# Kernel optimization log

Hardware: AMD Instinct MI355X
Metric: run time of the kernel (lower is better)

Reference implementation:

```python
import jax, jax.numpy as jnp
import numpy as np

EMB = 128
HID = 128
N = 1024


def setup_inputs() -> dict:
    key = jax.random.key(0)
    ks = jax.random.split(key, 10)
    s1 = 1.0 / np.sqrt(2 * EMB)
    s2 = 1.0 / np.sqrt(HID)
    return {
        "z1": jax.random.normal(ks[0], (N, EMB), jnp.float32),
        "z2": jax.random.normal(ks[1], (N, EMB), jnp.float32),
        "W1": jax.random.uniform(ks[2], (HID, 2 * EMB), jnp.float32, -s1, s1),
        "b1": jax.random.uniform(ks[3], (HID,), jnp.float32, -s1, s1),
        "W2": jax.random.uniform(ks[4], (HID, HID), jnp.float32, -s2, s2),
        "b2": jax.random.uniform(ks[5], (HID,), jnp.float32, -s2, s2),
        "W3": jax.random.uniform(ks[6], (1, HID), jnp.float32, -s2, s2),
        "b3": jax.random.uniform(ks[7], (1,), jnp.float32, -s2, s2),
    }


def reference(z1, z2, W1, b1, W2, b2, W3, b3):
    # pairs[i, j] = concat(z1[j], z2[i]); first Linear split into two matmuls
    # so the [n, n, 2*emb] concat tensor is never materialized (same math).
    W1a = W1[:, :EMB]   # acts on z1 half
    W1b = W1[:, EMB:]   # acts on z2 half
    a = jnp.einsum('jd,hd->jh', z1, W1a)          # [n, h], varies along j
    b = jnp.einsum('id,hd->ih', z2, W1b)          # [n, h], varies along i
    h1 = jax.nn.gelu(a[None, :, :] + b[:, None, :] + b1, approximate=False)  # [n, n, h]
    h2 = jax.nn.gelu(jnp.einsum('ijh,gh->ijg', h1, W2) + b2, approximate=False)
    log_q = jnp.einsum('ijh,oh->ijo', h2, W3) + b3  # [n, n, 1]
    return log_q[..., 0]
```

## Files before the change

kernel.cpp:

```cpp
#include <hip/hip_runtime.h>

#define NN  1024
#define EMB 128
#define HID 128

typedef __attribute__((ext_vector_type(4))) float float4v;
typedef __attribute__((ext_vector_type(8))) float float8v;
typedef __attribute__((ext_vector_type(8))) short short8;
typedef __attribute__((ext_vector_type(4))) __bf16 bf16x4;
typedef __attribute__((ext_vector_type(8))) __bf16 bf16x8;

__device__ __forceinline__ short8 to_bf16x8(float4v a, float4v b) {
  float8v f = {a[0], a[1], a[2], a[3], b[0], b[1], b[2], b[3]};
  bf16x8 r = __builtin_convertvector(f, bf16x8);
  return __builtin_bit_cast(short8, r);
}

__device__ __forceinline__ void store_bf16x4(short* p, float4v v) {
  bf16x4 r = __builtin_convertvector(v, bf16x4);
  *(bf16x4*)p = r;
}

__device__ __forceinline__ float4v gelu4(float4v x) {
  float4v x2 = x * x;
  float4v t = x2 * 0.1029432f + 2.3022086f;
  float4v y = x * t;
  float4v e;
  e[0] = __builtin_amdgcn_exp2f(y[0]);
  e[1] = __builtin_amdgcn_exp2f(y[1]);
  e[2] = __builtin_amdgcn_exp2f(y[2]);
  e[3] = __builtin_amdgcn_exp2f(y[3]);
  float4v d = e + 1.0f;
  float p01 = d[0] * d[1];
  float p23 = d[2] * d[3];
  float rall = __builtin_amdgcn_rcpf(p01 * p23);
  float r01 = p23 * rall;
  float r23 = p01 * rall;
  float4v rv;
  rv[0] = d[1] * r01;
  rv[1] = d[0] * r01;
  rv[2] = d[3] * r23;
  rv[3] = d[2] * r23;
  return x - x * rv;
}

__device__ __forceinline__ float4v mfma16(short8 a, short8 b, float4v c) {
  return __builtin_amdgcn_mfma_f32_16x16x32_bf16(a, b, c, 0, 0, 0);
}

__global__ __launch_bounds__(256)
void prep_kernel(const float* __restrict__ z1, const float* __restrict__ z2,
                 const float* __restrict__ W1, const float* __restrict__ b1,
                 const float* __restrict__ W2,
                 float* __restrict__ Abuf, float* __restrict__ Bbuf,
                 unsigned short* __restrict__ W2f) {
  int blk = blockIdx.x, tid = threadIdx.x;
  if (blk < 256) {
    int which = blk >> 7;
    int j0 = ((blk & 127) >> 1) << 4;
    int hh = blk & 1;
    const float* z = which ? z2 : z1;
    __shared__ __align__(16) short zf[4 * 64 * 8];
    __shared__ __align__(16) short w1f[16 * 64 * 8];

#pragma unroll
    for (int p = 0; p < 2; ++p) {
      int u = p * 256 + tid;
      int row = u >> 5;
      int c = (u & 31) * 4;
      float4v v = *(const float4v*)(z + (j0 + row) * EMB + c);
      int kt = c >> 5;
      int lane = ((c >> 3) & 3) * 16 + row;
      store_bf16x4(zf + (kt * 64 + lane) * 8 + (c & 7), v);
    }
    {
      const float* wbase = W1 + (hh * 64) * (2 * EMB) + which * EMB;
#pragma unroll
      for (int p = 0; p < 8; ++p) {
        int u = p * 256 + tid;
        int grow = u >> 5;
        int c = (u & 31) * 4;
        float4v v = *(const float4v*)(wbase + grow * (2 * EMB) + c);
        int kt = c >> 5;
        int ntl = grow >> 4;
        int lane = ((c >> 3) & 3) * 16 + (grow & 15);
        store_bf16x4(w1f + ((kt * 4 + ntl) * 64 + lane) * 8 + (c & 7), v);
      }
    }
    __syncthreads();

    int w = tid >> 6, l = tid & 63, r = l & 15, q = l >> 4;
    float4v acc = {};
#pragma unroll
    for (int kt = 0; kt < 4; ++kt) {
      short8 az = *(const short8*)(zf + (kt * 64 + l) * 8);
      short8 bf = *(const short8*)(w1f + ((kt * 4 + w) * 64 + l) * 8);
      acc = mfma16(az, bf, acc);
    }
    int gg = hh * 64 + w * 16 + r;
    float ba = which ? 0.0f : b1[gg];
    float* dstp = which ? Bbuf : Abuf;
#pragma unroll
    for (int reg = 0; reg < 4; ++reg)
      dstp[(j0 + q * 4 + reg) * HID + gg] = acc[reg] + ba;
  } else {
    int s0 = (blk - 256) * 2048 + tid * 8;
    float4v v0 = *(const float4v*)(W2 + s0);
    float4v v1 = *(const float4v*)(W2 + s0 + 4);
    float vals[8] = {v0[0], v0[1], v0[2], v0[3], v1[0], v1[1], v1[2], v1[3]};
#pragma unroll
    for (int j = 0; j < 8; ++j) {
      int s = s0 + j;
      int g = s >> 7;
      int h = s & 127;
      int kt = h >> 5;
      int nt = g >> 4;
      int lane = ((h >> 3) & 3) * 16 + (g & 15);
      int dst = ((kt * 8 + nt) * 64 + lane) * 8 + (h & 7);
      unsigned u = __float_as_uint(vals[j]);
      W2f[dst] = (unsigned short)((u + 0x7FFFu + ((u >> 16) & 1u)) >> 16);
    }
  }
}

__global__ __launch_bounds__(256, 4)
void fused_mlp_kernel(const float* __restrict__ Abuf, const float* __restrict__ Bbuf,
                      const float* __restrict__ W2f4,
                      const float* __restrict__ b2, const float* __restrict__ W3,
                      const float* __restrict__ b3, float* __restrict__ out) {
  __shared__ __align__(16) short s_w2[HID * HID];

  int tid = threadIdx.x;
  {
    const float4v* src = (const float4v*)W2f4;
    float4v* dst = (float4v*)s_w2;
#pragma unroll
    for (int t = 0; t < 8; ++t)
      dst[tid + t * 256] = src[tid + t * 256];
  }

  int w = tid >> 6, l = tid & 63, r = l & 15, q = l >> 4;
  int bi = (blockIdx.x >> 6) << 3;
  int bj = (blockIdx.x & 63) << 4;

  const float* Ap  = Abuf + (bj + r) * HID + q * 8;
  const float* Bp0 = Bbuf + (bi + 2 * w) * HID + q * 8;
  const float* Bp1 = Bp0 + HID;

  short8 afs[4][2];
  float4v s0 = {0.f, 0.f, 0.f, 0.f};
  float4v s1 = {0.f, 0.f, 0.f, 0.f};
  float4v acc[2][4];

  __syncthreads();

#pragma unroll
  for (int nt = 0; nt < 4; ++nt) {
    float4v bv = *(const float4v*)(b2 + nt * 16 + q * 4);
    acc[0][nt] = bv;
    acc[1][nt] = bv;
  }

  float4v a0  = *(const float4v*)(Ap);
  float4v a1  = *(const float4v*)(Ap + 4);
  float4v b00 = *(const float4v*)(Bp0);
  float4v b01 = *(const float4v*)(Bp0 + 4);
  float4v b10 = *(const float4v*)(Bp1);
  float4v b11 = *(const float4v*)(Bp1 + 4);

#pragma unroll
  for (int kt = 0; kt < 4; ++kt) {
    float4v ca0 = a0, ca1 = a1, cb00 = b00, cb01 = b01, cb10 = b10, cb11 = b11;
    if (kt < 3) {
      int off = (kt + 1) * 32;
      a0  = *(const float4v*)(Ap + off);
      a1  = *(const float4v*)(Ap + off + 4);
      b00 = *(const float4v*)(Bp0 + off);
      b01 = *(const float4v*)(Bp0 + off + 4);
      b10 = *(const float4v*)(Bp1 + off);
      b11 = *(const float4v*)(Bp1 + off + 4);
    }
    short8 af0 = to_bf16x8(gelu4(ca0 + cb00), gelu4(ca1 + cb01));
    short8 af1 = to_bf16x8(gelu4(ca0 + cb10), gelu4(ca1 + cb11));
    afs[kt][0] = af0;
    afs[kt][1] = af1;

    const short8* wrow = (const short8*)s_w2 + kt * 512 + l;
#pragma unroll
    for (int nt = 0; nt < 4; ++nt) {
      short8 wf = wrow[nt * 64];
      acc[0][nt] = mfma16(wf, af0, acc[0][nt]);
      acc[1][nt] = mfma16(wf, af1, acc[1][nt]);
    }
  }

#pragma unroll
  for (int nt = 0; nt < 4; ++nt) {
    float4v wv = *(const float4v*)(W3 + nt * 16 + q * 4);
    s0 = s0 + gelu4(acc[0][nt]) * wv;
    s1 = s1 + gelu4(acc[1][nt]) * wv;
  }

#pragma unroll
  for (int nt = 0; nt < 4; ++nt) {
    float4v bv = *(const float4v*)(b2 + (nt + 4) * 16 + q * 4);
    acc[0][nt] = bv;
    acc[1][nt] = bv;
  }
#pragma unroll
  for (int kt = 0; kt < 4; ++kt) {
    short8 af0 = afs[kt][0];
    short8 af1 = afs[kt][1];
    const short8* wrow = (const short8*)s_w2 + kt * 512 + 4 * 64 + l;
#pragma unroll
    for (int nt = 0; nt < 4; ++nt) {
      short8 wf = wrow[nt * 64];
      acc[0][nt] = mfma16(wf, af0, acc[0][nt]);
      acc[1][nt] = mfma16(wf, af1, acc[1][nt]);
    }
  }
#pragma unroll
  for (int nt = 0; nt < 4; ++nt) {
    float4v wv = *(const float4v*)(W3 + (nt + 4) * 16 + q * 4);
    s0 = s0 + gelu4(acc[0][nt]) * wv;
    s1 = s1 + gelu4(acc[1][nt]) * wv;
  }

  float bias3 = b3[0];
  float sc0 = s0[0] + s0[1] + s0[2] + s0[3];
  float sc1 = s1[0] + s1[1] + s1[2] + s1[3];
  sc0 += __shfl_xor(sc0, 16, 64);
  sc0 += __shfl_xor(sc0, 32, 64);
  sc1 += __shfl_xor(sc1, 16, 64);
  sc1 += __shfl_xor(sc1, 32, 64);
  if (l < 16) {
    out[(bi + 2 * w) * NN + bj + l]     = sc0 + bias3;
    out[(bi + 2 * w + 1) * NN + bj + l] = sc1 + bias3;
  }
}

extern "C" void kernel_launch(void* const* d_in, const int* in_sizes, int n_in,
                              void* d_out, int out_size, void* d_ws, size_t ws_size,
                              hipStream_t stream) {
  const float* z1 = (const float*)d_in[0];
  const float* z2 = (const float*)d_in[1];
  const float* W1 = (const float*)d_in[2];
  const float* b1 = (const float*)d_in[3];
  const float* W2 = (const float*)d_in[4];
  const float* b2 = (const float*)d_in[5];
  const float* W3 = (const float*)d_in[6];
  const float* b3 = (const float*)d_in[7];
  float* out = (float*)d_out;

  float* Abuf = (float*)d_ws;
  float* Bbuf = Abuf + NN * HID;
  unsigned short* W2f = (unsigned short*)(Bbuf + NN * HID);

  prep_kernel<<<264, 256, 0, stream>>>(z1, z2, W1, b1, W2, Abuf, Bbuf, W2f);
  fused_mlp_kernel<<<(NN / 8) * (NN / 16), 256, 0, stream>>>(
      Abuf, Bbuf, (const float*)W2f, b2, W3, b3, out);
}
```

Before: 160.9 us.

## Load W2 tiles straight into LDS and reorder W2 fragment layout by half

The W2 copy from global memory into shared memory now uses direct global-to-LDS loads instead of a register round-trip. The prep kernel lays out W2 fragments so that output columns 0-63 and 64-127 occupy separate contiguous halves, and the MLP kernel's indexing is updated to match. The manual software prefetch of the A/B activations is removed, leaving each k-step to load its own values. This trims registers and copy instructions and lets the first half of W2 be consumed on its own, at the cost of exposing activation load latency.

Result: no change. 158.9 us (-1.2%).

```diff
diff --git a/kernel.cpp b/kernel.cpp
--- a/kernel.cpp
+++ b/kernel.cpp
@@ -115,8 +115,9 @@
       int h = s & 127;
       int kt = h >> 5;
       int nt = g >> 4;
+      int p = nt >> 2;
       int lane = ((h >> 3) & 3) * 16 + (g & 15);
-      int dst = ((kt * 8 + nt) * 64 + lane) * 8 + (h & 7);
+      int dst = p * 8192 + ((kt * 4 + (nt & 3)) * 64 + lane) * 8 + (h & 7);
       unsigned u = __float_as_uint(vals[j]);
       W2f[dst] = (unsigned short)((u + 0x7FFFu + ((u >> 16) & 1u)) >> 16);
     }
@@ -131,15 +132,20 @@
   __shared__ __align__(16) short s_w2[HID * HID];
 
   int tid = threadIdx.x;
+  int w = tid >> 6, l = tid & 63, r = l & 15, q = l >> 4;
+
   {
-    const float4v* src = (const float4v*)W2f4;
-    float4v* dst = (float4v*)s_w2;
-#pragma unroll
-    for (int t = 0; t < 8; ++t)
-      dst[tid + t * 256] = src[tid + t * 256];
-  }
-
-  int w = tid >> 6, l = tid & 63, r = l & 15, q = l >> 4;
+    const float4v* wsrc = (const float4v*)W2f4;
+    int wb = tid & 192;
+#pragma unroll
+    for (int t = 0; t < 8; ++t) {
+      __builtin_amdgcn_global_load_lds(
+          (const __attribute__((address_space(1))) void*)(wsrc + t * 256 + tid),
+          (__attribute__((address_space(3))) void*)(s_w2 + (t * 256 + wb) * 8),
+          16, 0, 0);
+    }
+  }
+
   int bi = (blockIdx.x >> 6) << 3;
   int bj = (blockIdx.x & 63) << 4;
 
@@ -161,31 +167,22 @@
     acc[1][nt] = bv;
   }
 
-  float4v a0  = *(const float4v*)(Ap);
-  float4v a1  = *(const float4v*)(Ap + 4);
-  float4v b00 = *(const float4v*)(Bp0);
-  float4v b01 = *(const float4v*)(Bp0 + 4);
-  float4v b10 = *(const float4v*)(Bp1);
-  float4v b11 = *(const float4v*)(Bp1 + 4);
-
 #pragma unroll
   for (int kt = 0; kt < 4; ++kt) {
-    float4v ca0 = a0, ca1 = a1, cb00 = b00, cb01 = b01, cb10 = b10, cb11 = b11;
-    if (kt < 3) {
-      int off = (kt + 1) * 32;
-      a0  = *(const float4v*)(Ap + off);
-      a1  = *(const float4v*)(Ap + off + 4);
-      b00 = *(const float4v*)(Bp0 + off);
-      b01 = *(const float4v*)(Bp0 + off + 4);
-      b10 = *(const float4v*)(Bp1 + off);
-      b11 = *(const float4v*)(Bp1 + off + 4);
-    }
+    int off = kt * 32;
+    float4v ca0  = *(const float4v*)(Ap + off);
+    float4v ca1  = *(const float4v*)(Ap + off + 4);
+    float4v cb00 = *(const float4v*)(Bp0 + off);
+    float4v cb01 = *(const float4v*)(Bp0 + off + 4);
+    float4v cb10 = *(const float4v*)(Bp1 + off);
+    float4v cb11 = *(const float4v*)(Bp1 + off + 4);
+
     short8 af0 = to_bf16x8(gelu4(ca0 + cb00), gelu4(ca1 + cb01));
     short8 af1 = to_bf16x8(gelu4(ca0 + cb10), gelu4(ca1 + cb11));
     afs[kt][0] = af0;
     afs[kt][1] = af1;
 
-    const short8* wrow = (const short8*)s_w2 + kt * 512 + l;
+    const short8* wrow = (const short8*)s_w2 + kt * 256 + l;
 #pragma unroll
     for (int nt = 0; nt < 4; ++nt) {
       short8 wf = wrow[nt * 64];
@@ -211,7 +208,7 @@
   for (int kt = 0; kt < 4; ++kt) {
     short8 af0 = afs[kt][0];
     short8 af1 = afs[kt][1];
-    const short8* wrow = (const short8*)s_w2 + kt * 512 + 4 * 64 + l;
+    const short8* wrow = (const short8*)s_w2 + 1024 + kt * 256 + l;
 #pragma unroll
     for (int nt = 0; nt < 4; ++nt) {
       short8 wf = wrow[nt * 64];
```

## Load W2 into LDS via direct global_load_lds and pack GELU as float2 ops

Applied to the files above, without the earlier changes.

Replaces the register-staged copy of the pre-swizzled W2 fragments into shared memory with direct global-to-LDS loads, and reorders the W2 fragment layout in the prep kernel so each output-half's tiles are contiguous. The GELU helper and accumulators are restructured into float2 pieces so the compiler can emit packed FP32 instructions. The intent is to cut VGPR pressure and instruction count in the load prologue and the GELU-heavy inner loop. It relies on the per-wave LDS base addressing of global_load_lds matching the layout, and on the compiler actually emitting packed math.

Measured after the change: 157.3 us. 2.2% less time.

```diff
diff --git a/kernel.cpp b/kernel.cpp
--- a/kernel.cpp
+++ b/kernel.cpp
@@ -4,14 +4,18 @@
 #define EMB 128
 #define HID 128
 
+typedef __attribute__((ext_vector_type(2))) float float2v;
 typedef __attribute__((ext_vector_type(4))) float float4v;
 typedef __attribute__((ext_vector_type(8))) float float8v;
 typedef __attribute__((ext_vector_type(8))) short short8;
 typedef __attribute__((ext_vector_type(4))) __bf16 bf16x4;
 typedef __attribute__((ext_vector_type(8))) __bf16 bf16x8;
 
-__device__ __forceinline__ short8 to_bf16x8(float4v a, float4v b) {
-  float8v f = {a[0], a[1], a[2], a[3], b[0], b[1], b[2], b[3]};
+__device__ __forceinline__ float2v lo2(float4v v) { float2v r; r[0] = v[0]; r[1] = v[1]; return r; }
+__device__ __forceinline__ float2v hi2(float4v v) { float2v r; r[0] = v[2]; r[1] = v[3]; return r; }
+
+__device__ __forceinline__ short8 to_bf16x8_pk(float2v al, float2v ah, float2v bl, float2v bh) {
+  float8v f = {al[0], al[1], ah[0], ah[1], bl[0], bl[1], bh[0], bh[1]};
   bf16x8 r = __builtin_convertvector(f, bf16x8);
   return __builtin_bit_cast(short8, r);
 }
@@ -21,27 +25,33 @@
   *(bf16x4*)p = r;
 }
 
-__device__ __forceinline__ float4v gelu4(float4v x) {
-  float4v x2 = x * x;
-  float4v t = x2 * 0.1029432f + 2.3022086f;
-  float4v y = x * t;
-  float4v e;
-  e[0] = __builtin_amdgcn_exp2f(y[0]);
-  e[1] = __builtin_amdgcn_exp2f(y[1]);
-  e[2] = __builtin_amdgcn_exp2f(y[2]);
-  e[3] = __builtin_amdgcn_exp2f(y[3]);
-  float4v d = e + 1.0f;
-  float p01 = d[0] * d[1];
-  float p23 = d[2] * d[3];
+__device__ __forceinline__ void gelu4pk(float2v xl, float2v xh,
+                                        float2v& ol, float2v& oh) {
+  float2v x2l = xl * xl;
+  float2v x2h = xh * xh;
+  float2v tl = x2l * 0.1029432f + 2.3022086f;
+  float2v th = x2h * 0.1029432f + 2.3022086f;
+  float2v yl = xl * tl;
+  float2v yh = xh * th;
+  float2v el, eh;
+  el[0] = __builtin_amdgcn_exp2f(yl[0]);
+  el[1] = __builtin_amdgcn_exp2f(yl[1]);
+  eh[0] = __builtin_amdgcn_exp2f(yh[0]);
+  eh[1] = __builtin_amdgcn_exp2f(yh[1]);
+  float2v dl = el + 1.0f;
+  float2v dh = eh + 1.0f;
+  float p01 = dl[0] * dl[1];
+  float p23 = dh[0] * dh[1];
   float rall = __builtin_amdgcn_rcpf(p01 * p23);
   float r01 = p23 * rall;
   float r23 = p01 * rall;
-  float4v rv;
-  rv[0] = d[1] * r01;
-  rv[1] = d[0] * r01;
-  rv[2] = d[3] * r23;
-  rv[3] = d[2] * r23;
-  return x - x * rv;
+  float2v rvl, rvh;
+  rvl[0] = dl[1] * r01;
+  rvl[1] = dl[0] * r01;
+  rvh[0] = dh[1] * r23;
+  rvh[1] = dh[0] * r23;
+  ol = xl - xl * rvl;
+  oh = xh - xh * rvh;
 }
 
 __device__ __forceinline__ float4v mfma16(short8 a, short8 b, float4v c) {
@@ -115,8 +125,9 @@
       int h = s & 127;
       int kt = h >> 5;
       int nt = g >> 4;
+      int p = nt >> 2;
       int lane = ((h >> 3) & 3) * 16 + (g & 15);
-      int dst = ((kt * 8 + nt) * 64 + lane) * 8 + (h & 7);
+      int dst = p * 8192 + ((kt * 4 + (nt & 3)) * 64 + lane) * 8 + (h & 7);
       unsigned u = __float_as_uint(vals[j]);
       W2f[dst] = (unsigned short)((u + 0x7FFFu + ((u >> 16) & 1u)) >> 16);
     }
@@ -131,15 +142,20 @@
   __shared__ __align__(16) short s_w2[HID * HID];
 
   int tid = threadIdx.x;
+  int w = tid >> 6, l = tid & 63, r = l & 15, q = l >> 4;
+
   {
-    const float4v* src = (const float4v*)W2f4;
-    float4v* dst = (float4v*)s_w2;
-#pragma unroll
-    for (int t = 0; t < 8; ++t)
-      dst[tid + t * 256] = src[tid + t * 256];
-  }
-
-  int w = tid >> 6, l = tid & 63, r = l & 15, q = l >> 4;
+    const float4v* wsrc = (const float4v*)W2f4;
+    int wb = tid & 192;
+#pragma unroll
+    for (int t = 0; t < 8; ++t) {
+      __builtin_amdgcn_global_load_lds(
+          (const __attribute__((address_space(1))) void*)(wsrc + t * 256 + tid),
+          (__attribute__((address_space(3))) void*)(s_w2 + (t * 256 + wb) * 8),
+          16, 0, 0);
+    }
+  }
+
   int bi = (blockIdx.x >> 6) << 3;
   int bj = (blockIdx.x & 63) << 4;
 
@@ -148,8 +164,8 @@
   const float* Bp1 = Bp0 + HID;
 
   short8 afs[4][2];
-  float4v s0 = {0.f, 0.f, 0.f, 0.f};
-  float4v s1 = {0.f, 0.f, 0.f, 0.f};
+  float2v s0l = {0.f, 0.f}, s0h = {0.f, 0.f};
+  float2v s1l = {0.f, 0.f}, s1h = {0.f, 0.f};
   float4v acc[2][4];
 
   __syncthreads();
@@ -180,12 +196,17 @@
       b10 = *(const float4v*)(Bp1 + off);
       b11 = *(const float4v*)(Bp1 + off + 4);
     }
-    short8 af0 = to_bf16x8(gelu4(ca0 + cb00), gelu4(ca1 + cb01));
-    short8 af1 = to_bf16x8(gelu4(ca0 + cb10), gelu4(ca1 + cb11));
+    float2v g0l, g0h, g1l, g1h;
+    gelu4pk(lo2(ca0) + lo2(cb00), hi2(ca0) + hi2(cb00), g0l, g0h);
+    gelu4pk(lo2(ca1) + lo2(cb01), hi2(ca1) + hi2(cb01), g1l, g1h);
+    short8 af0 = to_bf16x8_pk(g0l, g0h, g1l, g1h);
+    gelu4pk(lo2(ca0) + lo2(cb10), hi2(ca0) + hi2(cb10), g0l, g0h);
+    gelu4pk(lo2(ca1) + lo2(cb11), hi2(ca1) + hi2(cb11), g1l, g1h);
+    short8 af1 = to_bf16x8_pk(g0l, g0h, g1l, g1h);
     afs[kt][0] = af0;
     afs[kt][1] = af1;
 
-    const short8* wrow = (const short8*)s_w2 + kt * 512 + l;
+    const short8* wrow = (const short8*)s_w2 + kt * 256 + l;
 #pragma unroll
     for (int nt = 0; nt < 4; ++nt) {
       short8 wf = wrow[nt * 64];
@@ -197,8 +218,13 @@
 #pragma unroll
   for (int nt = 0; nt < 4; ++nt) {
     float4v wv = *(const float4v*)(W3 + nt * 16 + q * 4);
-    s0 = s0 + gelu4(acc[0][nt]) * wv;
-    s1 = s1 + gelu4(acc[1][nt]) * wv;
+    float2v g0l, g0h, g1l, g1h;
+    gelu4pk(lo2(acc[0][nt]), hi2(acc[0][nt]), g0l, g0h);
+    gelu4pk(lo2(acc[1][nt]), hi2(acc[1][nt]), g1l, g1h);
+    s0l = s0l + g0l * lo2(wv);
+    s0h = s0h + g0h * hi2(wv);
+    s1l = s1l + g1l * lo2(wv);
+    s1h = s1h + g1h * hi2(wv);
   }
 
 #pragma unroll
@@ -211,7 +237,7 @@
   for (int kt = 0; kt < 4; ++kt) {
     short8 af0 = afs[kt][0];
     short8 af1 = afs[kt][1];
-    const short8* wrow = (const short8*)s_w2 + kt * 512 + 4 * 64 + l;
+    const short8* wrow = (const short8*)s_w2 + 1024 + kt * 256 + l;
 #pragma unroll
     for (int nt = 0; nt < 4; ++nt) {
       short8 wf = wrow[nt * 64];
@@ -222,13 +248,18 @@
 #pragma unroll
   for (int nt = 0; nt < 4; ++nt) {
     float4v wv = *(const float4v*)(W3 + (nt + 4) * 16 + q * 4);
-    s0 = s0 + gelu4(acc[0][nt]) * wv;
-    s1 = s1 + gelu4(acc[1][nt]) * wv;
+    float2v g0l, g0h, g1l, g1h;
+    gelu4pk(lo2(acc[0][nt]), hi2(acc[0][nt]), g0l, g0h);
+    gelu4pk(lo2(acc[1][nt]), hi2(acc[1][nt]), g1l, g1h);
+    s0l = s0l + g0l * lo2(wv);
+    s0h = s0h + g0h * hi2(wv);
+    s1l = s1l + g1l * lo2(wv);
+    s1h = s1h + g1h * hi2(wv);
   }
 
   float bias3 = b3[0];
-  float sc0 = s0[0] + s0[1] + s0[2] + s0[3];
-  float sc1 = s1[0] + s1[1] + s1[2] + s1[3];
+  float sc0 = s0l[0] + s0l[1] + s0h[0] + s0h[1];
+  float sc1 = s1l[0] + s1l[1] + s1h[0] + s1h[1];
   sc0 += __shfl_xor(sc0, 16, 64);
   sc0 += __shfl_xor(sc0, 32, 64);
   sc1 += __shfl_xor(sc1, 16, 64);
```
